# Optimization experiments

Measured on AMD Instinct MI355X. Metric: run time of the kernel, lower is better.

The kernel has to match this reference:

```python
import jax, jax.numpy as jnp
import numpy as np

N = 50000      # nodes
E = 1600000    # edges (avg degree 32)
H = 2          # num_heads
F = 32         # att_feat
IN = 32        # in_feats (must equal att_feat, see w1(h_dst + g))
OUT = 32       # out_feats
NEG_SLOPE = 0.2


def setup_inputs() -> dict:
    key = jax.random.key(0)
    ks = jax.random.split(key, 11)
    s = 0.1  # param init scale
    return {
        "feat": jax.random.normal(ks[0], (N, IN), jnp.float32),
        "r_feat": jax.random.normal(ks[1], (E, H, F), jnp.float32),
        "src": jax.random.randint(ks[2], (E,), 0, N),
        "dst": jax.random.randint(ks[3], (E,), 0, N),
        "W1": jax.random.normal(ks[4], (IN, OUT), jnp.float32) * s,
        "b1": jnp.zeros((OUT,), jnp.float32),
        "W2s": jax.random.normal(ks[5], (IN, H * F), jnp.float32) * s,
        "b2s": jnp.zeros((H * F,), jnp.float32),
        "W2d": jax.random.normal(ks[6], (IN, H * F), jnp.float32) * s,
        "b2d": jnp.zeros((H * F,), jnp.float32),
        "attn": jax.random.normal(ks[7], (1, H, F), jnp.float32) * s,
    }


def reference(feat, r_feat, src, dst, W1, b1, W2s, b2s, W2d, b2d, attn):
    n = feat.shape[0]
    # projections (dropout = 0 -> identity)
    feat_src = (feat @ W2s + b2s).reshape(n, H, F)   # [N,H,F]
    feat_dst = (feat @ W2d + b2d).reshape(n, H, F)   # [N,H,F]
    en = feat_src[src]                                # [E,H,F] gather
    ev = feat_dst[dst]                                # [E,H,F] gather
    # u_add_v + leaky_relu, dot with attention vector
    e = jax.nn.leaky_relu(en + ev, negative_slope=NEG_SLOPE)
    e = jnp.sum(e * attn, axis=-1, keepdims=True)     # [E,H,1]
    # edge_softmax: softmax over incoming edges of each dst node
    m = jax.ops.segment_max(e, dst, num_segments=n)   # [N,H,1]
    m = jnp.where(jnp.isfinite(m), m, 0.0)            # zero in-degree -> -inf
    ee = jnp.exp(e - m[dst])                          # [E,H,1]
    denom = jax.ops.segment_sum(ee, dst, num_segments=n)
    alpha = ee / jnp.maximum(denom[dst], 1e-9)        # [E,H,1]
    # message: softmax over feature dim of (en * rr * alpha)
    msg = jax.nn.softmax(en * r_feat * alpha, axis=-1)  # [E,H,F]
    g_agg = jax.ops.segment_sum(msg, dst, num_segments=n)  # [N,H,F]
    g_sum = jnp.sum(g_agg, axis=1)                    # att_agg='sum' -> [N,F]
    rst = (feat + g_sum) @ W1 + b1                    # [N,OUT]
    return rst
```

## Files before the change

### kernel.cpp

```cpp
#include <hip/hip_runtime.h>

#define N_NODES 50000
#define E_EDGES 1600000
#define NHEAD 2
#define FDIM 32
#define HF 64
#define IN_F 32
#define OUT_F 32
#define CAPB 128

__device__ __forceinline__ int rl(int v, int l) { return __builtin_amdgcn_readlane(v, l); }

template<int CTRL>
__device__ __forceinline__ float dpp_add(float v) {
    int t = __builtin_amdgcn_update_dpp(0, __float_as_int(v), CTRL, 0xf, 0xf, true);
    return v + __int_as_float(t);
}
__device__ __forceinline__ float red4_sum(float v) {
    v = dpp_add<0xB1>(v);
    v = dpp_add<0x4E>(v);
    return v;
}
template<int PAT>
__device__ __forceinline__ float swz_add(float v) {
    return v + __int_as_float(__builtin_amdgcn_ds_swizzle(__float_as_int(v), PAT));
}
__device__ __forceinline__ float red64_sum(float v) {
    v = red4_sum(v);
    v = swz_add<0x101F>(v);
    v = swz_add<0x201F>(v);
    v = swz_add<0x401F>(v);
    v += __shfl_xor(v, 32, 64);
    return v;
}
__device__ __forceinline__ void load8(float* d, const float* __restrict__ p) {
    *(float4*)&d[0] = *(const float4*)&p[0];
    *(float4*)&d[4] = *(const float4*)&p[4];
}

__global__ void proj_kernel(const float* __restrict__ feat,
                            const float* __restrict__ W2s, const float* __restrict__ b2s,
                            const float* __restrict__ W2d, const float* __restrict__ b2d,
                            float* __restrict__ fsrc, float* __restrict__ fdst,
                            int* __restrict__ cur) {
    int idx = blockIdx.x * blockDim.x + threadIdx.x;
    int n = idx >> 6;
    int c = idx & 63;
    if (n >= N_NODES) return;
    if (c == 0) cur[n] = 0;
    const float* frow = feat + n * IN_F;
    float s = b2s[c];
    float d = b2d[c];
    #pragma unroll
    for (int k = 0; k < IN_F; ++k) {
        float fv = frow[k];
        s += fv * W2s[k * HF + c];
        d += fv * W2d[k * HF + c];
    }
    fsrc[n * HF + c] = s;
    fdst[n * HF + c] = d;
}

__global__ void scatter_kernel(const int4* __restrict__ src4, const int4* __restrict__ dst4,
                               int* __restrict__ cur, int2* __restrict__ pairs) {
    int i = blockIdx.x * blockDim.x + threadIdx.x;
    if (i * 4 < E_EDGES) {
        int4 s = src4[i];
        int4 d = dst4[i];
        int e = 4 * i;
        int p0 = atomicAdd(&cur[d.x], 1);
        if (p0 < CAPB) pairs[(size_t)d.x * CAPB + p0] = make_int2(s.x, e + 0);
        int p1 = atomicAdd(&cur[d.y], 1);
        if (p1 < CAPB) pairs[(size_t)d.y * CAPB + p1] = make_int2(s.y, e + 1);
        int p2 = atomicAdd(&cur[d.z], 1);
        if (p2 < CAPB) pairs[(size_t)d.z * CAPB + p2] = make_int2(s.z, e + 2);
        int p3 = atomicAdd(&cur[d.w], 1);
        if (p3 < CAPB) pairs[(size_t)d.w * CAPB + p3] = make_int2(s.w, e + 3);
    }
}

__global__ __launch_bounds__(256) void agg_kernel(
        const int* __restrict__ cur, const int2* __restrict__ pairs,
        const float* __restrict__ fsrc, const float* __restrict__ fdst,
        const float* __restrict__ rfeat, const float* __restrict__ attn,
        const float* __restrict__ feat,
        const float* __restrict__ W1, const float* __restrict__ b1,
        float* __restrict__ out) {
    __shared__ float denL[2][NHEAD];
    __shared__ __align__(16) float gpart[2][NHEAD][FDIM];
    int tid = threadIdx.x;
    int wib = tid >> 6;
    int h  = wib & 1;
    int gr = wib >> 1;
    int n = blockIdx.x;
    int lane = tid & 63;
    int eL = lane >> 2;
    int q = lane & 3;
    int deg = min(cur[n], CAPB);
    const int2* bucket = pairs + (size_t)n * CAPB;

    int hq = h * FDIM + q * 8;
    float ev[8], aw[8];
    load8(ev, fdst + n * HF + hq);
    load8(aw, attn + hq);

    int2 se[2];
    float en[2][8];
    #pragma unroll
    for (int j = 0; j < 2; ++j) {
        int idx = gr * 32 + j * 16 + eL;
        se[j] = make_int2(0, 0);
        if (idx < deg) se[j] = bucket[idx];
        load8(en[j], fsrc + se[j].x * HF + hq);
    }
    float E[2];
    float denp = 0.0f;
    #pragma unroll
    for (int j = 0; j < 2; ++j) {
        float acc = 0.0f;
        #pragma unroll
        for (int k = 0; k < 8; ++k) {
            float x = en[j][k] + ev[k];
            x = fmaxf(x, 0.2f * x);
            acc = fmaf(x, aw[k], acc);
        }
        float v = red4_sum(acc);
        E[j] = (gr * 32 + j * 16 + eL < deg) ? __expf(v) : 0.0f;
        denp += E[j];
    }
    if (deg > 64) {
        for (int b = 64 + gr * 16; b < deg; b += 32) {
            int idx = b + eL;
            int2 se2 = make_int2(0, 0);
            if (idx < deg) se2 = bucket[idx];
            float en2[8];
            load8(en2, fsrc + se2.x * HF + hq);
            float acc = 0.0f;
            #pragma unroll
            for (int k = 0; k < 8; ++k) {
                float x = en2[k] + ev[k];
                x = fmaxf(x, 0.2f * x);
                acc = fmaf(x, aw[k], acc);
            }
            float v = red4_sum(acc);
            denp += (idx < deg) ? __expf(v) : 0.0f;
        }
    }
    float denw = red64_sum(denp) * 0.25f;
    if (lane == 0) denL[gr][h] = denw;

    float r[2][8];
    #pragma unroll
    for (int j = 0; j < 2; ++j)
        load8(r[j], rfeat + (size_t)se[j].y * HF + hq);

    __syncthreads();
    float den = denL[0][h] + denL[1][h];
    float dinv = __builtin_amdgcn_rcpf(fmaxf(den, 1e-9f));

    float g[8] = {0, 0, 0, 0, 0, 0, 0, 0};
    #pragma unroll
    for (int j = 0; j < 2; ++j) {
        float a = E[j] * dinv;
        float p[8];
        float S = 0.0f;
        #pragma unroll
        for (int k = 0; k < 8; ++k) {
            p[k] = __expf(en[j][k] * r[j][k] * a);
            S += p[k];
        }
        S = red4_sum(S);
        float w = (gr * 32 + j * 16 + eL < deg) ? __builtin_amdgcn_rcpf(S) : 0.0f;
        #pragma unroll
        for (int k = 0; k < 8; ++k) g[k] = fmaf(p[k], w, g[k]);
    }
    if (deg > 64) {
        for (int b = 64 + gr * 16; b < deg; b += 32) {
            int idx = b + eL;
            int2 se2 = make_int2(0, 0);
            if (idx < deg) se2 = bucket[idx];
            float en2[8], r2[8], p[8];
            load8(en2, fsrc + se2.x * HF + hq);
            load8(r2, rfeat + (size_t)se2.y * HF + hq);
            float acc = 0.0f;
            #pragma unroll
            for (int k = 0; k < 8; ++k) {
                float x = en2[k] + ev[k];
                x = fmaxf(x, 0.2f * x);
                acc = fmaf(x, aw[k], acc);
            }
            float v = red4_sum(acc);
            float a = ((idx < deg) ? __expf(v) : 0.0f) * dinv;
            float S = 0.0f;
            #pragma unroll
            for (int k = 0; k < 8; ++k) {
                p[k] = __expf(en2[k] * r2[k] * a);
                S += p[k];
            }
            S = red4_sum(S);
            float w = (idx < deg) ? __builtin_amdgcn_rcpf(S) : 0.0f;
            #pragma unroll
            for (int k = 0; k < 8; ++k) g[k] = fmaf(p[k], w, g[k]);
        }
    }

    #pragma unroll
    for (int k = 0; k < 8; ++k) {
        float v = g[k];
        v = swz_add<0x101F>(v);
        v = swz_add<0x201F>(v);
        v = swz_add<0x401F>(v);
        v += __shfl_xor(v, 32, 64);
        g[k] = v;
    }
    if (lane < 4) {
        *(float4*)&gpart[gr][h][lane * 8]     = make_float4(g[0], g[1], g[2], g[3]);
        *(float4*)&gpart[gr][h][lane * 8 + 4] = make_float4(g[4], g[5], g[6], g[7]);
    }
    __syncthreads();

    if (wib == 0) {
        int f = lane & 31;
        float gs = (gpart[0][0][f] + gpart[0][1][f]) + (gpart[1][0][f] + gpart[1][1][f]);
        float x = feat[n * IN_F + f] + gs;
        float acc = b1[f];
        #pragma unroll
        for (int k = 0; k < 32; ++k) {
            float xk = __int_as_float(rl(__float_as_int(x), k));
            acc = fmaf(xk, W1[k * OUT_F + f], acc);
        }
        if (lane < 32) out[n * OUT_F + f] = acc;
    }
}

extern "C" void kernel_launch(void* const* d_in, const int* in_sizes, int n_in,
                              void* d_out, int out_size, void* d_ws, size_t ws_size,
                              hipStream_t stream) {
    const float* feat  = (const float*)d_in[0];
    const float* rfeat = (const float*)d_in[1];
    const int*   src   = (const int*)d_in[2];
    const int*   dst   = (const int*)d_in[3];
    const float* W1    = (const float*)d_in[4];
    const float* b1    = (const float*)d_in[5];
    const float* W2s   = (const float*)d_in[6];
    const float* b2s   = (const float*)d_in[7];
    const float* W2d   = (const float*)d_in[8];
    const float* b2d   = (const float*)d_in[9];
    const float* attn  = (const float*)d_in[10];
    float* out = (float*)d_out;

    float* fsrc = (float*)d_ws;
    float* fdst = fsrc + (size_t)N_NODES * HF;
    int*   cur  = (int*)(fdst + (size_t)N_NODES * HF);
    int2*  pairs = (int2*)(cur + N_NODES);

    const int BLK = 256;
    proj_kernel<<<(N_NODES * HF + BLK - 1) / BLK, BLK, 0, stream>>>(
        feat, W2s, b2s, W2d, b2d, fsrc, fdst, cur);
    scatter_kernel<<<(E_EDGES / 4 + BLK - 1) / BLK, BLK, 0, stream>>>(
        (const int4*)src, (const int4*)dst, cur, pairs);
    agg_kernel<<<N_NODES, BLK, 0, stream>>>(
        cur, pairs, fsrc, fdst, rfeat, attn, feat, W1, b1, out);
}
```

Measured before the change: 285.0 us.

## Process two nodes per block and stage rfeat rows into LDS via async loads

```diff
diff --git a/kernel.cpp b/kernel.cpp
--- a/kernel.cpp
+++ b/kernel.cpp
@@ -86,37 +86,48 @@
         const float* __restrict__ feat,
         const float* __restrict__ W1, const float* __restrict__ b1,
         float* __restrict__ out) {
-    __shared__ float denL[2][NHEAD];
+    __shared__ __align__(16) float rfeatL[2][64][64];
     __shared__ __align__(16) float gpart[2][NHEAD][FDIM];
     int tid = threadIdx.x;
     int wib = tid >> 6;
+    int nb = wib >> 1;
     int h  = wib & 1;
-    int gr = wib >> 1;
-    int n = blockIdx.x;
+    int n = blockIdx.x * 2 + nb;
     int lane = tid & 63;
     int eL = lane >> 2;
     int q = lane & 3;
     int deg = min(cur[n], CAPB);
     const int2* bucket = pairs + (size_t)n * CAPB;
 
+    int2 es = (lane < deg) ? bucket[lane] : make_int2(0, 0);
+
     int hq = h * FDIM + q * 8;
     float ev[8], aw[8];
     load8(ev, fdst + n * HF + hq);
     load8(aw, attn + hq);
 
-    int2 se[2];
-    float en[2][8];
-    #pragma unroll
-    for (int j = 0; j < 2; ++j) {
-        int idx = gr * 32 + j * 16 + eL;
-        se[j] = make_int2(0, 0);
-        if (idx < deg) se[j] = bucket[idx];
-        load8(en[j], fsrc + se[j].x * HF + hq);
-    }
-    float E[2];
+    float en[4][8];
+    #pragma unroll
+    for (int j = 0; j < 4; ++j) {
+        int idx = j * 16 + eL;
+        int sx = __shfl(es.x, idx, 64);
+        load8(en[j], fsrc + sx * HF + hq);
+    }
+
+    int c16 = lane & 15;
+    int rsub = lane >> 4;
+    #pragma unroll
+    for (int j2 = 0; j2 < 8; ++j2) {
+        int idxs = h * 32 + j2 * 4 + rsub;
+        int eid = __shfl(es.y, idxs, 64);
+        const float* gsrc = rfeat + (size_t)eid * HF + ((c16 ^ (idxs & 6)) << 2);
+        __builtin_amdgcn_global_load_lds(gsrc, &rfeatL[nb][h * 32 + j2 * 4][0], 16, 0, 0);
+    }
+
+    float E[4];
     float denp = 0.0f;
     #pragma unroll
-    for (int j = 0; j < 2; ++j) {
+    for (int j = 0; j < 4; ++j) {
         float acc = 0.0f;
         #pragma unroll
         for (int k = 0; k < 8; ++k) {
@@ -125,11 +136,11 @@
             acc = fmaf(x, aw[k], acc);
         }
         float v = red4_sum(acc);
-        E[j] = (gr * 32 + j * 16 + eL < deg) ? __expf(v) : 0.0f;
+        E[j] = (j * 16 + eL < deg) ? __expf(v) : 0.0f;
         denp += E[j];
     }
     if (deg > 64) {
-        for (int b = 64 + gr * 16; b < deg; b += 32) {
+        for (int b = 64; b < deg; b += 16) {
             int idx = b + eL;
             int2 se2 = make_int2(0, 0);
             if (idx < deg) se2 = bucket[idx];
@@ -146,36 +157,36 @@
             denp += (idx < deg) ? __expf(v) : 0.0f;
         }
     }
-    float denw = red64_sum(denp) * 0.25f;
-    if (lane == 0) denL[gr][h] = denw;
-
-    float r[2][8];
-    #pragma unroll
-    for (int j = 0; j < 2; ++j)
-        load8(r[j], rfeat + (size_t)se[j].y * HF + hq);
-
+    float den = red64_sum(denp) * 0.25f;
+    float dinv = __builtin_amdgcn_rcpf(fmaxf(den, 1e-9f));
+
+    asm volatile("s_waitcnt vmcnt(0)" ::: "memory");
     __syncthreads();
-    float den = denL[0][h] + denL[1][h];
-    float dinv = __builtin_amdgcn_rcpf(fmaxf(den, 1e-9f));
 
     float g[8] = {0, 0, 0, 0, 0, 0, 0, 0};
     #pragma unroll
-    for (int j = 0; j < 2; ++j) {
+    for (int j = 0; j < 4; ++j) {
+        int idx = j * 16 + eL;
+        int cbase = ((h * 8 + 2 * q) ^ (idx & 6)) << 2;
+        const float* rp = &rfeatL[nb][idx][cbase];
+        float r[8];
+        *(float4*)&r[0] = *(const float4*)&rp[0];
+        *(float4*)&r[4] = *(const float4*)&rp[4];
         float a = E[j] * dinv;
         float p[8];
         float S = 0.0f;
         #pragma unroll
         for (int k = 0; k < 8; ++k) {
-            p[k] = __expf(en[j][k] * r[j][k] * a);
+            p[k] = __expf(en[j][k] * r[k] * a);
             S += p[k];
         }
         S = red4_sum(S);
-        float w = (gr * 32 + j * 16 + eL < deg) ? __builtin_amdgcn_rcpf(S) : 0.0f;
+        float w = (idx < deg) ? __builtin_amdgcn_rcpf(S) : 0.0f;
         #pragma unroll
         for (int k = 0; k < 8; ++k) g[k] = fmaf(p[k], w, g[k]);
     }
     if (deg > 64) {
-        for (int b = 64 + gr * 16; b < deg; b += 32) {
+        for (int b = 64; b < deg; b += 16) {
             int idx = b + eL;
             int2 se2 = make_int2(0, 0);
             if (idx < deg) se2 = bucket[idx];
@@ -214,14 +225,14 @@
         g[k] = v;
     }
     if (lane < 4) {
-        *(float4*)&gpart[gr][h][lane * 8]     = make_float4(g[0], g[1], g[2], g[3]);
-        *(float4*)&gpart[gr][h][lane * 8 + 4] = make_float4(g[4], g[5], g[6], g[7]);
+        *(float4*)&gpart[nb][h][lane * 8]     = make_float4(g[0], g[1], g[2], g[3]);
+        *(float4*)&gpart[nb][h][lane * 8 + 4] = make_float4(g[4], g[5], g[6], g[7]);
     }
     __syncthreads();
 
-    if (wib == 0) {
+    if (h == 0) {
         int f = lane & 31;
-        float gs = (gpart[0][0][f] + gpart[0][1][f]) + (gpart[1][0][f] + gpart[1][1][f]);
+        float gs = gpart[nb][0][f] + gpart[nb][1][f];
         float x = feat[n * IN_F + f] + gs;
         float acc = b1[f];
         #pragma unroll
@@ -259,6 +270,6 @@
         feat, W2s, b2s, W2d, b2d, fsrc, fdst, cur);
     scatter_kernel<<<(E_EDGES / 4 + BLK - 1) / BLK, BLK, 0, stream>>>(
         (const int4*)src, (const int4*)dst, cur, pairs);
-    agg_kernel<<<N_NODES, BLK, 0, stream>>>(
+    agg_kernel<<<N_NODES / 2, BLK, 0, stream>>>(
         cur, pairs, fsrc, fdst, rfeat, attn, feat, W1, b1, out);
 }
```

After: 320.9 us. 1.13x slower.
